# Performance work log

Measured on AMD Instinct MI355X. Metric: run time of the kernel, lower is better.

Reference implementation:

```python
import jax, jax.numpy as jnp
import numpy as np

# Dimensions (babyGPT-50m: GPT-2-small-ish)
B, T, V, C, H, L = 2, 1024, 50257, 768, 12, 6
D = C // H
STD = 0.02
EPS = 1e-5


def _normal(k, shape):
    return (jax.random.normal(k, shape, dtype=jnp.float32) * STD)


def setup_inputs() -> dict:
    key = jax.random.key(0)
    ks = jax.random.split(key, 12)
    inp = {
        "idx": jax.random.randint(ks[0], (B, T), 0, V, dtype=jnp.int64 if jax.config.jax_enable_x64 else jnp.int32),
        "tok_emb": _normal(ks[1], (V, C)),
        "pos_emb": _normal(ks[2], (1, T, C)),
        # per-layer params stacked along leading L axis
        "ln1_g": jnp.ones((L, C), jnp.float32),
        "ln1_b": jnp.zeros((L, C), jnp.float32),
        "Wq": _normal(ks[3], (L, C, C)), "bq": jnp.zeros((L, C), jnp.float32),
        "Wk": _normal(ks[4], (L, C, C)), "bk": jnp.zeros((L, C), jnp.float32),
        "Wv": _normal(ks[5], (L, C, C)), "bv": jnp.zeros((L, C), jnp.float32),
        "Wp": _normal(ks[6], (L, C, C)), "bp": jnp.zeros((L, C), jnp.float32),
        "ln2_g": jnp.ones((L, C), jnp.float32),
        "ln2_b": jnp.zeros((L, C), jnp.float32),
        "Wf1": _normal(ks[7], (L, C, 4 * C)), "bf1": jnp.zeros((L, 4 * C), jnp.float32),
        "Wf2": _normal(ks[8], (L, 4 * C, C)), "bf2": jnp.zeros((L, C), jnp.float32),
        "lnf_g": jnp.ones((C,), jnp.float32),
        "lnf_b": jnp.zeros((C,), jnp.float32),
        "head_W": _normal(ks[9], (C, V)),  # head has bias=False
    }
    return inp


def _ln(x, g, b):
    m = jnp.mean(x, axis=-1, keepdims=True)
    v = jnp.var(x, axis=-1, keepdims=True)
    return (x - m) * jax.lax.rsqrt(v + EPS) * g + b


def _gpt_forward(idx, tok_emb, pos_emb, ln1_g, ln1_b, Wq, bq, Wk, bk, Wv, bv,
                 Wp, bp, ln2_g, ln2_b, Wf1, bf1, Wf2, bf2, lnf_g, lnf_b, head_W):
    x = tok_emb[idx] + pos_emb[:, :T]          # [B,T,C]; dropout is identity (eval)
    causal = jnp.tril(jnp.ones((T, T), bool))  # same tril mask as the buffer
    scale = 1.0 / np.sqrt(D).astype(np.float32)

    def block(x, p):
        g1, b1, wq, bq_, wk, bk_, wv, bv_, wp, bp_, g2, b2, w1, b1f, w2, b2f = p
        h = _ln(x, g1, b1)
        q = (h @ wq + bq_).reshape(B, T, H, D)
        k = (h @ wk + bk_).reshape(B, T, H, D)
        v = (h @ wv + bv_).reshape(B, T, H, D)
        att = jnp.einsum('bthd,bshd->bhts', q, k) * scale   # [B,H,T,T]
        att = jnp.where(causal, att, jnp.float32(-10000.0))  # masked_fill value
        att = jax.nn.softmax(att, axis=-1)
        y = jnp.einsum('bhts,bshd->bthd', att, v).reshape(B, T, C)
        x = x + y @ wp + bp_
        h2 = _ln(x, g2, b2)
        ff = jax.nn.gelu(h2 @ w1 + b1f, approximate=False) @ w2 + b2f  # exact GELU, dropout=eval
        return x + ff, None

    layer_params = (ln1_g, ln1_b, Wq, bq, Wk, bk, Wv, bv, Wp, bp,
                    ln2_g, ln2_b, Wf1, bf1, Wf2, bf2)
    x, _ = jax.lax.scan(block, x, layer_params)
    x = _ln(x, lnf_g, lnf_b)
    return x @ head_W  # logits [B,T,V]


def reference(idx, tok_emb, pos_emb, ln1_g, ln1_b, Wq, bq, Wk, bk, Wv, bv,
              Wp, bp, ln2_g, ln2_b, Wf1, bf1, Wf2, bf2, lnf_g, lnf_b, head_W):
    return _gpt_forward(idx, tok_emb, pos_emb, ln1_g, ln1_b, Wq, bq, Wk, bk, Wv, bv,
                        Wp, bp, ln2_g, ln2_b, Wf1, bf1, Wf2, bf2, lnf_g, lnf_b, head_W)
```

## Files before the change

kernel.cpp:

```cpp
#include <hip/hip_runtime.h>
#include <hip/hip_bf16.h>
#include <math.h>

#define Bsz 2
#define Tt 1024
#define Vv 50257
#define Cc 768
#define Hh 12
#define Ll 6
#define NTOK (Bsz*Tt)
#define VPAD 50304

typedef __attribute__((ext_vector_type(8))) short bf16x8;
typedef __attribute__((ext_vector_type(8))) unsigned short u16x8;
typedef __attribute__((ext_vector_type(4))) unsigned short u16x4;
typedef __attribute__((ext_vector_type(4))) float f32x4;
typedef unsigned short u16;

static __device__ __forceinline__ u16 f2bf(float f){
  unsigned u = __float_as_uint(f);
  u += 0x7FFF + ((u >> 16) & 1);
  return (u16)(u >> 16);
}
static __device__ __forceinline__ float bf2f(u16 h){
  return __uint_as_float(((unsigned)h) << 16);
}

#define GL16(g,l) __builtin_amdgcn_global_load_lds( \
    (const __attribute__((address_space(1))) void*)(g), \
    (__attribute__((address_space(3))) void*)(l), 16, 0, 0)
#define WAITVM(n) asm volatile("s_waitcnt vmcnt(%0)" :: "n"(n) : "memory")

__global__ void embed_kernel(const int* __restrict__ idx, const float* __restrict__ tok,
                             const float* __restrict__ pos, float* __restrict__ x){
  const int C4 = Cc/4;
  int i = blockIdx.x * 256 + threadIdx.x;
  if (i >= NTOK*C4) return;
  int tk = i / C4, c4 = i % C4;
  int row = idx[tk];
  int t = tk % Tt;
  float4 a = ((const float4*)tok)[(size_t)row*C4 + c4];
  float4 p = ((const float4*)pos)[(size_t)t*C4 + c4];
  float4 r; r.x=a.x+p.x; r.y=a.y+p.y; r.z=a.z+p.z; r.w=a.w+p.w;
  ((float4*)x)[i] = r;
}

__global__ void ln_kernel(const float* __restrict__ in, const float* __restrict__ g,
                          const float* __restrict__ bt, u16* __restrict__ out){
  int row = blockIdx.x, tid = threadIdx.x;
  const float* r = in + (size_t)row*Cc;
  float v0=r[tid], v1=r[tid+256], v2=r[tid+512];
  float s  = v0+v1+v2;
  float s2 = v0*v0+v1*v1+v2*v2;
  #pragma unroll
  for (int off=32; off; off>>=1){ s += __shfl_xor(s,off); s2 += __shfl_xor(s2,off); }
  __shared__ float red[8];
  int wid = tid >> 6;
  if ((tid & 63) == 0){ red[wid]=s; red[4+wid]=s2; }
  __syncthreads();
  float S  = red[0]+red[1]+red[2]+red[3];
  float S2 = red[4]+red[5]+red[6]+red[7];
  float mean = S * (1.0f/Cc);
  float var  = S2 * (1.0f/Cc) - mean*mean;
  float rstd = rsqrtf(var + 1e-5f);
  u16* o = out + (size_t)row*Cc;
  o[tid]     = f2bf((v0-mean)*rstd*g[tid]     + bt[tid]);
  o[tid+256] = f2bf((v1-mean)*rstd*g[tid+256] + bt[tid+256]);
  o[tid+512] = f2bf((v2-mean)*rstd*g[tid+512] + bt[tid+512]);
}

__global__ void wtrans_kernel(const float* __restrict__ in, u16* __restrict__ out,
                              int K, int N, int Npad, size_t lsi, size_t lso){
  __shared__ float t[64][33];
  const float* inp = in + (size_t)blockIdx.z*lsi;
  u16* op = out + (size_t)blockIdx.z*lso;
  int n0 = blockIdx.x*32, k0 = blockIdx.y*64;
  int tx = threadIdx.x, ty = threadIdx.y;
  #pragma unroll
  for (int i=0;i<8;i++){
    int k = k0+ty+i*8, n = n0+tx;
    t[ty+i*8][tx] = (n < N) ? inp[(size_t)k*N + n] : 0.f;
  }
  __syncthreads();
  #pragma unroll
  for (int i=0;i<2;i++){
    int nl = i*16 + ty*2 + (tx>>4);
    int kl = (tx&15)*4;
    int n = n0 + nl;
    if (n < Npad){
      u16x4 pk;
      pk[0] = f2bf(t[kl+0][nl]); pk[1] = f2bf(t[kl+1][nl]);
      pk[2] = f2bf(t[kl+2][nl]); pk[3] = f2bf(t[kl+3][nl]);
      *(u16x4*)&op[(size_t)n*K + k0 + kl] = pk;
    }
  }
}

__global__ void vtrans_kernel(const u16* __restrict__ qkv, u16* __restrict__ vT){
  __shared__ u16 s[32][33];
  int bh = blockIdx.z; int b = bh/Hh, h = bh - b*Hh;
  int t0 = blockIdx.x*32, d0 = blockIdx.y*32;
  int tx=threadIdx.x, ty=threadIdx.y;
  #pragma unroll
  for (int i=0;i<4;i++)
    s[ty+i*8][tx] = qkv[(size_t)(b*Tt + t0+ty+i*8)*2304 + 1536 + h*64 + d0 + tx];
  __syncthreads();
  #pragma unroll
  for (int i=0;i<4;i++)
    vT[((size_t)bh*64 + d0+ty+i*8)*Tt + t0 + tx] = s[tx][ty+i*8];
}

__global__ void bconcat_kernel(const float* __restrict__ bq, const float* __restrict__ bk,
                               const float* __restrict__ bv, float* __restrict__ o){
  int i = blockIdx.x*256 + threadIdx.x;
  if (i >= Ll*2304) return;
  int l = i/2304, j = i - l*2304;
  o[i] = (j < 768) ? bq[l*768+j] : (j < 1536) ? bk[l*768+j-768] : bv[l*768+j-1536];
}

__global__ __launch_bounds__(256) void flash_kernel(
    const u16* __restrict__ qkv, const u16* __restrict__ vT, u16* __restrict__ y){
  __shared__ u16 Ks[2][64*64];
  __shared__ u16 Vs[2][64*64];
  __shared__ u16 Ps[4][16*64];
  int bx = blockIdx.x;
  int bh = blockIdx.y; int b = bh/Hh, h = bh - b*Hh;
  int q0 = bx*64;
  int tid = threadIdx.x, lane = tid&63, wid = tid>>6;
  const size_t tokbase = (size_t)b*Tt;
  int arow = lane&15, akof = (lane>>4)*8;
  bf16x8 qa[2];
  #pragma unroll
  for (int ks=0;ks<2;ks++)
    qa[ks] = *(const bf16x8*)&qkv[(tokbase + q0 + wid*16 + arow)*2304
                                  + h*64 + ks*32 + akof];
  int srow = lane>>3;
  int sbyte = ((lane&7)*16) ^ (srow<<4);
  const u16* kbase = qkv + tokbase*2304 + 768 + h*64;
  const u16* vbase = vT + (size_t)bh*64*Tt;
  auto STAGEKV = [&](int t, int bb){
    int j0 = t*64;
    #pragma unroll
    for (int c=0;c<2;c++){
      int r = wid*16 + c*8 + srow;
      GL16(kbase + (size_t)(j0 + r)*2304 + (sbyte>>1), &Ks[bb][(wid*16 + c*8)*64]);
      GL16(vbase + (size_t)r*Tt + j0 + (sbyte>>1),     &Vs[bb][(wid*16 + c*8)*64]);
    }
  };
  float m_r[4], l_r[4];
  f32x4 o_acc[4] = {};
  #pragma unroll
  for (int jj=0;jj<4;jj++){ m_r[jj] = -1e30f; l_r[jj] = 0.f; }

  int njt = bx + 1;
  STAGEKV(0, 0);
  asm volatile("s_waitcnt vmcnt(0)" ::: "memory");
  __builtin_amdgcn_s_barrier();
  for (int t=0; t<njt; t++){
    int cur = t&1;
    if (t+1 < njt) STAGEKV(t+1, cur^1);
    int j0 = t*64;
    f32x4 sacc[4] = {};
    #pragma unroll
    for (int ks=0;ks<2;ks++){
      bf16x8 kf[4];
      #pragma unroll
      for (int ni=0;ni<4;ni++){
        int s16 = ni*16 + (lane&15);
        int kb = (ks*64 + (lane>>4)*16) ^ ((s16&7)<<4);
        kf[ni] = *(const bf16x8*)((const char*)&Ks[cur][0] + s16*128 + kb);
      }
      #pragma unroll
      for (int ni=0;ni<4;ni++)
        sacc[ni] = __builtin_amdgcn_mfma_f32_16x16x32_bf16(qa[ks], kf[ni], sacc[ni], 0,0,0);
    }
    float tmax[4];
    #pragma unroll
    for (int jj=0;jj<4;jj++) tmax[jj] = -1e30f;
    #pragma unroll
    for (int ni=0;ni<4;ni++)
      #pragma unroll
      for (int jj=0;jj<4;jj++){
        float v = sacc[ni][jj]*0.125f;
        int sg = j0 + ni*16 + (lane&15);
        int tg = q0 + wid*16 + (lane>>4)*4 + jj;
        v = (sg <= tg) ? v : -1e30f;
        sacc[ni][jj] = v;
        tmax[jj] = fmaxf(tmax[jj], v);
      }
    #pragma unroll
    for (int jj=0;jj<4;jj++){
      float tm = tmax[jj];
      tm = fmaxf(tm, __shfl_xor(tm,1)); tm = fmaxf(tm, __shfl_xor(tm,2));
      tm = fmaxf(tm, __shfl_xor(tm,4)); tm = fmaxf(tm, __shfl_xor(tm,8));
      float mn = fmaxf(m_r[jj], tm);
      float al = __expf(m_r[jj] - mn);
      m_r[jj] = mn;
      l_r[jj] *= al;
      tmax[jj] = al;
    }
    float tsum[4] = {};
    #pragma unroll
    for (int ni=0;ni<4;ni++)
      #pragma unroll
      for (int jj=0;jj<4;jj++){
        float p = __expf(sacc[ni][jj] - m_r[jj]);
        tsum[jj] += p;
        int pr = (lane>>4)*4 + jj;
        int pcb = (2*(ni*16 + (lane&15))) ^ ((pr&7)<<4);
        *(u16*)((char*)&Ps[wid][0] + pr*128 + pcb) = f2bf(p);
      }
    #pragma unroll
    for (int jj=0;jj<4;jj++){
      float ts = tsum[jj];
      ts += __shfl_xor(ts,1); ts += __shfl_xor(ts,2);
      ts += __shfl_xor(ts,4); ts += __shfl_xor(ts,8);
      l_r[jj] += ts;
      float al = tmax[jj];
      #pragma unroll
      for (int ni2=0;ni2<4;ni2++) o_acc[ni2][jj] *= al;
    }
    #pragma unroll
    for (int ks2=0;ks2<2;ks2++){
      bf16x8 pa, vf[4];
      int prr = lane&15;
      int pb = (ks2*64 + (lane>>4)*16) ^ ((prr&7)<<4);
      pa = *(const bf16x8*)((const char*)&Ps[wid][0] + prr*128 + pb);
      #pragma unroll
      for (int ni2=0;ni2<4;ni2++){
        int d16 = ni2*16 + (lane&15);
        int sb = (ks2*64 + (lane>>4)*16) ^ ((d16&7)<<4);
        vf[ni2] = *(const bf16x8*)((const char*)&Vs[cur][0] + d16*128 + sb);
      }
      #pragma unroll
      for (int ni2=0;ni2<4;ni2++)
        o_acc[ni2] = __builtin_amdgcn_mfma_f32_16x16x32_bf16(pa, vf[ni2], o_acc[ni2], 0,0,0);
    }
    asm volatile("s_waitcnt vmcnt(0) lgkmcnt(0)" ::: "memory");
    __builtin_amdgcn_s_barrier();
  }
  #pragma unroll
  for (int jj=0;jj<4;jj++){
    float inv = 1.0f / l_r[jj];
    int tok2 = q0 + wid*16 + (lane>>4)*4 + jj;
    size_t rb = (tokbase + tok2)*Cc + h*64;
    #pragma unroll
    for (int ni2=0;ni2<4;ni2++)
      y[rb + ni2*16 + (lane&15)] = f2bf(o_acc[ni2][jj] * inv);
  }
}

template<int NBUF, int BM, int BN, bool BIAS, bool RESID, bool GELU, bool OUTBF, bool ROWSCAN>
__global__ __launch_bounds__(256) void mm_kernel(
    const u16* __restrict__ A, const u16* __restrict__ Bm,
    const float* __restrict__ bias, const float* __restrict__ resid,
    void* __restrict__ out, int N, int K, int lda, int ldb, int ldc)
{
  constexpr int FM   = BM/32;
  constexpr int FN   = BN/32;
  constexpr int CPW  = FN*16;
  constexpr int ESTR = CPW + 4;
  constexpr int ABUF = BM*64;
  constexpr int BBUF = BN*64;
  constexpr int ACALLS = BM/32;
  constexpr int BCALLS = BN/32;
  constexpr int LOADS = ACALLS + BCALLS;
  constexpr int SMEM_STAGE = NBUF*(ABUF+BBUF)*2;
  constexpr int SMEM_EPI   = 4*16*ESTR*4;
  constexpr int SMEMB = SMEM_STAGE > SMEM_EPI ? SMEM_STAGE : SMEM_EPI;
  __shared__ __align__(16) char smem[SMEMB];
  u16* As = (u16*)smem;
  u16* Bs = As + NBUF*ABUF;

  int bx = blockIdx.x, by = blockIdx.y;
  {
    int gx = gridDim.x;
    int nwg = gx * gridDim.y;
    int flat = by*gx + bx;
    int qq = nwg >> 3, rr = nwg & 7;
    int xcd = flat & 7, lid = flat >> 3;
    int swz = (xcd < rr) ? xcd*(qq+1) + lid : rr*(qq+1) + (xcd-rr)*qq + lid;
    bx = swz % gx; by = swz / gx;
  }
  int m0 = bx*BM, n0 = by*BN;
  int tid = threadIdx.x, lane = tid & 63, wid = tid >> 6;
  int wr = wid >> 1, wc = wid & 1;
  int r0 = wr*(BM/2), c0 = wc*(BN/2);
  int lrow = lane & 15;
  int sswz = ((lane & 7) ^ (lane >> 3)) * 8;
  const u16* Ap = A + (size_t)(m0 + wid*(BM/4) + (lane>>3))*lda + sswz;
  const u16* Bp = Bm + (size_t)(n0 + wid*(BN/4) + (lane>>3))*ldb + sswz;
  int cof0 = (((lane>>4)    ) ^ (lane&7)) << 4;
  int cof1 = (((lane>>4) + 4) ^ (lane&7)) << 4;
  int nt = K/64;
  auto STAGE = [&](int t, int bb){
    int kk = t*64;
    u16* Albase = As + bb*ABUF + (wid*(BM/4))*64;
    #pragma unroll
    for (int c=0;c<ACALLS;c++)
      GL16(Ap + kk + (size_t)(c*8)*lda, Albase + c*512);
    u16* Blbase = Bs + bb*BBUF + (wid*(BN/4))*64;
    #pragma unroll
    for (int c=0;c<BCALLS;c++)
      GL16(Bp + kk + (size_t)(c*8)*ldb, Blbase + c*512);
  };
  f32x4 acc[FM][FN] = {};
  if constexpr (NBUF==2){
    STAGE(0, 0);
    WAITVM(0);
    __builtin_amdgcn_s_barrier();
  } else {
    STAGE(0, 0);
    if (nt > 1) STAGE(1, 1);
    WAITVM(LOADS);
    __builtin_amdgcn_s_barrier();
  }
  for (int t = 0; t < nt; t++){
    int bb = (NBUF==2) ? (t & 1) : (t % 3);
    if constexpr (NBUF==2){
      if (t+1 < nt) STAGE(t+1, (t+1)&1);
    } else {
      if (t+2 < nt) STAGE(t+2, (t+2)%3);
    }
    const char* Ab2 = (const char*)(As + bb*ABUF);
    const char* Bb2 = (const char*)(Bs + bb*BBUF);
    #pragma unroll
    for (int ks=0;ks<2;ks++){
      int cof = ks ? cof1 : cof0;
      bf16x8 af[FM], bfr[FN];
      #pragma unroll
      for (int m=0;m<FM;m++) af[m] = *(const bf16x8*)(Ab2 + (r0 + m*16 + lrow)*128 + cof);
      #pragma unroll
      for (int n=0;n<FN;n++) bfr[n] = *(const bf16x8*)(Bb2 + (c0 + n*16 + lrow)*128 + cof);
      #pragma unroll
      for (int m=0;m<FM;m++)
        #pragma unroll
        for (int n=0;n<FN;n++)
          acc[m][n] = __builtin_amdgcn_mfma_f32_16x16x32_bf16(af[m], bfr[n], acc[m][n], 0,0,0);
    }
    if constexpr (NBUF==2){
      asm volatile("s_waitcnt vmcnt(0) lgkmcnt(0)" ::: "memory");
    } else {
      if (t+2 < nt) WAITVM(LOADS); else WAITVM(0);
    }
    __builtin_amdgcn_s_barrier();
  }

  float* ebuf = (float*)smem + wid*16*ESTR;
  int er = lane >> 2;
  int ec = (lane & 3) * (CPW/4);
  #pragma unroll
  for (int m=0;m<FM;m++){
    #pragma unroll
    for (int n=0;n<FN;n++)
      #pragma unroll
      for (int j=0;j<4;j++)
        ebuf[((lane>>4)*4+j)*ESTR + n*16 + (lane&15)] = acc[m][n][j];
    __builtin_amdgcn_s_waitcnt(0);
    if constexpr (ROWSCAN){
      #pragma unroll
      for (int rr2=0; rr2<16; rr2++){
        int gr2 = m0 + r0 + m*16 + rr2;
        int gc2 = n0 + c0 + lane;
        float v = ebuf[rr2*ESTR + lane];
        if (gc2 < N)
          __builtin_nontemporal_store(v, &((float*)out)[(size_t)gr2*ldc + gc2]);
      }
    } else {
      int grow = m0 + r0 + m*16 + er;
      int gcol = n0 + c0 + ec;
      size_t rbase = (size_t)grow*ldc;
      if constexpr (OUTBF){
        u16 tmp[CPW/4];
        #pragma unroll
        for (int q=0;q<FN;q++){
          float4 v = *(const float4*)&ebuf[er*ESTR + ec + q*4];
          float f0=v.x, f1=v.y, f2=v.z, f3=v.w;
          if (BIAS){
            float4 b4 = *(const float4*)&bias[gcol + q*4];
            f0+=b4.x; f1+=b4.y; f2+=b4.z; f3+=b4.w;
          }
          if (GELU){
            f0 = 0.5f*f0*(1.f+erff(f0*0.70710678118654752f));
            f1 = 0.5f*f1*(1.f+erff(f1*0.70710678118654752f));
            f2 = 0.5f*f2*(1.f+erff(f2*0.70710678118654752f));
            f3 = 0.5f*f3*(1.f+erff(f3*0.70710678118654752f));
          }
          tmp[q*4+0]=f2bf(f0); tmp[q*4+1]=f2bf(f1);
          tmp[q*4+2]=f2bf(f2); tmp[q*4+3]=f2bf(f3);
        }
        #pragma unroll
        for (int s2=0; s2<CPW/32; s2++)
          *(u16x8*)&((u16*)out)[rbase + gcol + s2*8] = *(const u16x8*)&tmp[s2*8];
      } else {
        #pragma unroll
        for (int q=0;q<FN;q++){
          float4 v = *(const float4*)&ebuf[er*ESTR + ec + q*4];
          float f0=v.x, f1=v.y, f2=v.z, f3=v.w;
          if (BIAS){
            float4 b4 = *(const float4*)&bias[gcol + q*4];
            f0+=b4.x; f1+=b4.y; f2+=b4.z; f3+=b4.w;
          }
          if (GELU){
            f0 = 0.5f*f0*(1.f+erff(f0*0.70710678118654752f));
            f1 = 0.5f*f1*(1.f+erff(f1*0.70710678118654752f));
            f2 = 0.5f*f2*(1.f+erff(f2*0.70710678118654752f));
            f3 = 0.5f*f3*(1.f+erff(f3*0.70710678118654752f));
          }
          if (RESID){
            float4 r4 = *(const float4*)&resid[rbase + gcol + q*4];
            f0+=r4.x; f1+=r4.y; f2+=r4.z; f3+=r4.w;
          }
          float4 o4; o4.x=f0; o4.y=f1; o4.z=f2; o4.w=f3;
          *(float4*)&((float*)out)[rbase + gcol + q*4] = o4;
        }
      }
    }
  }
}

extern "C" void kernel_launch(void* const* d_in, const int* in_sizes, int n_in,
                              void* d_out, int out_size, void* d_ws, size_t ws_size,
                              hipStream_t stream){
  const int*   idx  = (const int*)d_in[0];
  const float* tok  = (const float*)d_in[1];
  const float* pos  = (const float*)d_in[2];
  const float* ln1g = (const float*)d_in[3];
  const float* ln1b = (const float*)d_in[4];
  const float* Wq   = (const float*)d_in[5];
  const float* bq   = (const float*)d_in[6];
  const float* Wk   = (const float*)d_in[7];
  const float* bk   = (const float*)d_in[8];
  const float* Wv   = (const float*)d_in[9];
  const float* bv   = (const float*)d_in[10];
  const float* Wp   = (const float*)d_in[11];
  const float* bp   = (const float*)d_in[12];
  const float* ln2g = (const float*)d_in[13];
  const float* ln2b = (const float*)d_in[14];
  const float* Wf1  = (const float*)d_in[15];
  const float* bf1  = (const float*)d_in[16];
  const float* Wf2  = (const float*)d_in[17];
  const float* bf2  = (const float*)d_in[18];
  const float* lnfg = (const float*)d_in[19];
  const float* lnfb = (const float*)d_in[20];
  const float* headW= (const float*)d_in[21];
  float* outp = (float*)d_out;

  char* w = (char*)d_ws;
  u16* wqkvT = (u16*)w;  w += (size_t)Ll*2304*768*2;
  u16* wpT   = (u16*)w;  w += (size_t)Ll*768*768*2;
  u16* wf1T  = (u16*)w;  w += (size_t)Ll*3072*768*2;
  u16* wf2T  = (u16*)w;  w += (size_t)Ll*768*3072*2;
  u16* headT = (u16*)w;  w += (size_t)VPAD*768*2;
  float* bqkv= (float*)w;w += (size_t)Ll*2304*4;
  float* x   = (float*)w;w += (size_t)NTOK*Cc*4;
  u16* h     = (u16*)w;  w += (size_t)NTOK*Cc*2;
  u16* qkv   = (u16*)w;  w += (size_t)NTOK*2304*2;
  u16* vT    = (u16*)w;  w += (size_t)Bsz*Hh*64*Tt*2;
  u16* y     = (u16*)w;  w += (size_t)NTOK*Cc*2;
  u16* ff    = (u16*)w;  w += (size_t)NTOK*4*Cc*2;

  dim3 tb(32,8);
  wtrans_kernel<<<dim3(24,12,Ll), tb, 0, stream>>>(Wq, wqkvT,          768, 768, 768, (size_t)Cc*Cc, (size_t)2304*768);
  wtrans_kernel<<<dim3(24,12,Ll), tb, 0, stream>>>(Wk, wqkvT+768*768,  768, 768, 768, (size_t)Cc*Cc, (size_t)2304*768);
  wtrans_kernel<<<dim3(24,12,Ll), tb, 0, stream>>>(Wv, wqkvT+1536*768, 768, 768, 768, (size_t)Cc*Cc, (size_t)2304*768);
  wtrans_kernel<<<dim3(24,12,Ll), tb, 0, stream>>>(Wp, wpT,            768, 768, 768, (size_t)Cc*Cc, (size_t)768*768);
  wtrans_kernel<<<dim3(96,12,Ll), tb, 0, stream>>>(Wf1, wf1T,          768, 3072, 3072, (size_t)Cc*4*Cc, (size_t)3072*768);
  wtrans_kernel<<<dim3(24,48,Ll), tb, 0, stream>>>(Wf2, wf2T,          3072, 768, 768, (size_t)4*Cc*Cc, (size_t)768*3072);
  wtrans_kernel<<<dim3(VPAD/32,12,1), tb, 0, stream>>>(headW, headT, 768, Vv, VPAD, 0, 0);
  bconcat_kernel<<<(Ll*2304+255)/256, 256, 0, stream>>>(bq, bk, bv, bqkv);

  embed_kernel<<<NTOK*(Cc/4)/256, 256, 0, stream>>>(idx, tok, pos, x);

  for (int l=0;l<Ll;l++){
    ln_kernel<<<NTOK, 256, 0, stream>>>(x, ln1g+l*Cc, ln1b+l*Cc, h);
    mm_kernel<2,64,128,true,false,false,true,false><<<dim3(32,18,1), 256, 0, stream>>>(
        h, wqkvT+(size_t)l*2304*768, bqkv+l*2304, nullptr, qkv, 2304, 768, 768, 768, 2304);
    vtrans_kernel<<<dim3(32,2,Bsz*Hh), tb, 0, stream>>>(qkv, vT);
    flash_kernel<<<dim3(Tt/64, Bsz*Hh), 256, 0, stream>>>(qkv, vT, y);
    mm_kernel<3,64,64,true,true,false,false,false><<<dim3(32,12,1), 256, 0, stream>>>(
        y, wpT+(size_t)l*768*768, bp+l*Cc, x, x, 768, 768, 768, 768, 768);
    ln_kernel<<<NTOK, 256, 0, stream>>>(x, ln2g+l*Cc, ln2b+l*Cc, h);
    mm_kernel<2,64,128,true,false,true,true,false><<<dim3(32,24,1), 256, 0, stream>>>(
        h, wf1T+(size_t)l*3072*768, bf1+(size_t)l*4*Cc, nullptr, ff, 3072, 768, 768, 768, 3072);
    mm_kernel<3,64,64,true,true,false,false,false><<<dim3(32,12,1), 256, 0, stream>>>(
        ff, wf2T+(size_t)l*768*3072, bf2+l*Cc, x, x, 768, 3072, 3072, 3072, 768);
  }
  ln_kernel<<<NTOK, 256, 0, stream>>>(x, lnfg, lnfb, h);
  mm_kernel<2,128,128,false,false,false,false,true><<<dim3(16,VPAD/128,1), 256, 0, stream>>>(
      h, headT, nullptr, nullptr, outp, Vv, 768, 768, 768, Vv);
}
```

Measured before the change: 1.148 ms.

## Generalize GEMM wave layout and use 512-thread 128x256 tiles for LM head

```diff
diff --git a/kernel.cpp b/kernel.cpp
--- a/kernel.cpp
+++ b/kernel.cpp
@@ -9,7 +9,7 @@
 #define Hh 12
 #define Ll 6
 #define NTOK (Bsz*Tt)
-#define VPAD 50304
+#define VPAD 50432
 
 typedef __attribute__((ext_vector_type(8))) short bf16x8;
 typedef __attribute__((ext_vector_type(8))) unsigned short u16x8;
@@ -250,23 +250,28 @@
   }
 }
 
-template<int NBUF, int BM, int BN, bool BIAS, bool RESID, bool GELU, bool OUTBF, bool ROWSCAN>
-__global__ __launch_bounds__(256) void mm_kernel(
+template<int NBUF, int NTHR, int WN, int BM, int BN,
+         bool BIAS, bool RESID, bool GELU, bool OUTBF, bool ROWSCAN>
+__global__ __launch_bounds__(NTHR) void mm_kernel(
     const u16* __restrict__ A, const u16* __restrict__ Bm,
     const float* __restrict__ bias, const float* __restrict__ resid,
     void* __restrict__ out, int N, int K, int lda, int ldb, int ldc)
 {
-  constexpr int FM   = BM/32;
-  constexpr int FN   = BN/32;
-  constexpr int CPW  = FN*16;
-  constexpr int ESTR = CPW + 4;
-  constexpr int ABUF = BM*64;
-  constexpr int BBUF = BN*64;
-  constexpr int ACALLS = BM/32;
-  constexpr int BCALLS = BN/32;
+  constexpr int WAVES = NTHR/64;
+  constexpr int WM    = WAVES/WN;
+  constexpr int FM    = BM/(WM*16);
+  constexpr int FN    = BN/(WN*16);
+  constexpr int CPW   = FN*16;
+  constexpr int ESTR  = CPW + 4;
+  constexpr int ABUF  = BM*64;
+  constexpr int BBUF  = BN*64;
+  constexpr int ARPW  = BM/WAVES;
+  constexpr int BRPW  = BN/WAVES;
+  constexpr int ACALLS = ARPW/8;
+  constexpr int BCALLS = BRPW/8;
   constexpr int LOADS = ACALLS + BCALLS;
   constexpr int SMEM_STAGE = NBUF*(ABUF+BBUF)*2;
-  constexpr int SMEM_EPI   = 4*16*ESTR*4;
+  constexpr int SMEM_EPI   = WAVES*16*ESTR*4;
   constexpr int SMEMB = SMEM_STAGE > SMEM_EPI ? SMEM_STAGE : SMEM_EPI;
   __shared__ __align__(16) char smem[SMEMB];
   u16* As = (u16*)smem;
@@ -284,25 +289,24 @@
   }
   int m0 = bx*BM, n0 = by*BN;
   int tid = threadIdx.x, lane = tid & 63, wid = tid >> 6;
-  int wr = wid >> 1, wc = wid & 1;
-  int r0 = wr*(BM/2), c0 = wc*(BN/2);
+  int r0 = (wid/WN)*(BM/WM), c0 = (wid%WN)*(BN/WN);
   int lrow = lane & 15;
   int sswz = ((lane & 7) ^ (lane >> 3)) * 8;
-  const u16* Ap = A + (size_t)(m0 + wid*(BM/4) + (lane>>3))*lda + sswz;
-  const u16* Bp = Bm + (size_t)(n0 + wid*(BN/4) + (lane>>3))*ldb + sswz;
+  const u16* Ap = A + (size_t)(m0 + wid*ARPW + (lane>>3))*lda + sswz;
+  const u16* Bp = Bm + (size_t)(n0 + wid*BRPW + (lane>>3))*ldb + sswz;
   int cof0 = (((lane>>4)    ) ^ (lane&7)) << 4;
   int cof1 = (((lane>>4) + 4) ^ (lane&7)) << 4;
   int nt = K/64;
   auto STAGE = [&](int t, int bb){
     int kk = t*64;
-    u16* Albase = As + bb*ABUF + (wid*(BM/4))*64;
+    u16* Al = As + bb*ABUF + (wid*ARPW)*64;
     #pragma unroll
     for (int c=0;c<ACALLS;c++)
-      GL16(Ap + kk + (size_t)(c*8)*lda, Albase + c*512);
-    u16* Blbase = Bs + bb*BBUF + (wid*(BN/4))*64;
+      GL16(Ap + kk + (size_t)(c*8)*lda, Al + c*512);
+    u16* Bl = Bs + bb*BBUF + (wid*BRPW)*64;
     #pragma unroll
     for (int c=0;c<BCALLS;c++)
-      GL16(Bp + kk + (size_t)(c*8)*ldb, Blbase + c*512);
+      GL16(Bp + kk + (size_t)(c*8)*ldb, Bl + c*512);
   };
   f32x4 acc[FM][FN] = {};
   if constexpr (NBUF==2){
@@ -474,19 +478,19 @@
 
   for (int l=0;l<Ll;l++){
     ln_kernel<<<NTOK, 256, 0, stream>>>(x, ln1g+l*Cc, ln1b+l*Cc, h);
-    mm_kernel<2,64,128,true,false,false,true,false><<<dim3(32,18,1), 256, 0, stream>>>(
+    mm_kernel<2,256,2,64,128,true,false,false,true,false><<<dim3(32,18,1), 256, 0, stream>>>(
         h, wqkvT+(size_t)l*2304*768, bqkv+l*2304, nullptr, qkv, 2304, 768, 768, 768, 2304);
     vtrans_kernel<<<dim3(32,2,Bsz*Hh), tb, 0, stream>>>(qkv, vT);
     flash_kernel<<<dim3(Tt/64, Bsz*Hh), 256, 0, stream>>>(qkv, vT, y);
-    mm_kernel<3,64,64,true,true,false,false,false><<<dim3(32,12,1), 256, 0, stream>>>(
+    mm_kernel<3,256,2,64,64,true,true,false,false,false><<<dim3(32,12,1), 256, 0, stream>>>(
         y, wpT+(size_t)l*768*768, bp+l*Cc, x, x, 768, 768, 768, 768, 768);
     ln_kernel<<<NTOK, 256, 0, stream>>>(x, ln2g+l*Cc, ln2b+l*Cc, h);
-    mm_kernel<2,64,128,true,false,true,true,false><<<dim3(32,24,1), 256, 0, stream>>>(
+    mm_kernel<2,256,2,64,128,true,false,true,true,false><<<dim3(32,24,1), 256, 0, stream>>>(
         h, wf1T+(size_t)l*3072*768, bf1+(size_t)l*4*Cc, nullptr, ff, 3072, 768, 768, 768, 3072);
-    mm_kernel<3,64,64,true,true,false,false,false><<<dim3(32,12,1), 256, 0, stream>>>(
+    mm_kernel<3,256,2,64,64,true,true,false,false,false><<<dim3(32,12,1), 256, 0, stream>>>(
         ff, wf2T+(size_t)l*768*3072, bf2+l*Cc, x, x, 768, 3072, 3072, 3072, 768);
   }
   ln_kernel<<<NTOK, 256, 0, stream>>>(x, lnfg, lnfb, h);
-  mm_kernel<2,128,128,false,false,false,false,true><<<dim3(16,VPAD/128,1), 256, 0, stream>>>(
+  mm_kernel<3,512,4,128,256,false,false,false,false,true><<<dim3(16,VPAD/256,1), 512, 0, stream>>>(
       h, headT, nullptr, nullptr, outp, Vv, 768, 768, 768, Vv);
 }
```

After: 1.150 ms. No clear change (+0.1%).
